# Kernel optimization log

Measured on AMD Instinct MI355X. Metric: run time of the kernel, lower is better.

## Reference

```python
import jax, jax.numpy as jnp
import numpy as np

N_TOKEN = 267735
HEAD = 20000
CUTOFFS = [20000, 20008, 20016, 200000, 267735]  # from cl_root_leaf_dict with 2 roots of 8 leaves
N_ROOTS = 2


def setup_inputs() -> dict:
    key = jax.random.key(0)
    k1, k2, k3, k4 = jax.random.split(key, 4)
    N, D = 1024, 1024
    hidden = jax.random.normal(k1, (N, D), dtype=jnp.float32)
    target = jax.random.randint(k2, (N,), 0, N_TOKEN)
    W = jax.random.normal(k3, (N_TOKEN, D), dtype=jnp.float32) * 0.02
    b = jnp.zeros((N_TOKEN,), dtype=jnp.float32)
    cluster_weight = jax.random.normal(k4, (2, D), dtype=jnp.float32) * 0.02
    cluster_bias = jnp.zeros((2,), dtype=jnp.float32)
    return {"hidden": hidden, "target": target, "W": W, "b": b,
            "cluster_weight": cluster_weight, "cluster_bias": cluster_bias}


def _nll(hidden, target, W, b, cw, cb):
    cutoff_ends = [0] + CUTOFFS
    # head = first 20000 vocab rows + 2 cluster rows (d_proj == d_embed -> no projection)
    head_w = jnp.concatenate([W[:HEAD], cw], axis=0)          # [20002, D]
    head_b = jnp.concatenate([b[:HEAD], cb], axis=0)          # [20002]
    head_lp = jax.nn.log_softmax(hidden @ head_w.T + head_b, axis=-1)  # [N, 20002]
    n_head_cols = head_lp.shape[1]
    rows = jnp.arange(hidden.shape[0])
    # segment 0: target in [0, 20000) -> nll directly from head log-probs
    lp0 = head_lp[rows, jnp.clip(target, 0, HEAD - 1)]
    nll = -lp0  # only valid where target < HEAD; overwritten below otherwise
    for i in range(1, len(CUTOFFS)):
        l, r = cutoff_ends[i], cutoff_ends[i + 1]
        # per-segment tail logits for all tokens (masked combine keeps shapes static)
        tail_lp = jax.nn.log_softmax(hidden @ W[l:r].T + b[l:r], axis=-1)  # [N, r-l]
        # routing column exactly as in the torch code:
        # j = i-1 for root segments, -(i - n_roots) for the two cluster segments
        j = (i - 1) if i <= N_ROOTS else (n_head_cols - (i - N_ROOTS))
        lp_i = head_lp[:, j] + tail_lp[rows, jnp.clip(target - l, 0, r - l - 1)]
        mask = (target >= l) & (target < r)
        nll = jnp.where(mask, -lp_i, nll)
    return nll


def reference(hidden, target, W, b, cluster_weight, cluster_bias):
    return _nll(hidden, target, W, b, cluster_weight, cluster_bias)
```

## Files before the change

kernel.cpp:

```cpp
#include <hip/hip_runtime.h>
#include <hip/hip_bf16.h>

#define D_DIM 1024
#define NTOK 267735
#define NEXT_ 267737
#define HEADN 20000

typedef __attribute__((ext_vector_type(8))) short bf16x8;
typedef __attribute__((ext_vector_type(4))) float f32x4;
typedef __attribute__((ext_vector_type(4))) unsigned uint4v;

__device__ __forceinline__ int seg_of(int c){
  if (c < HEADN)  return 0;
  if (c < 20008)  return 1;
  if (c < 20016)  return 2;
  if (c < 200000) return 3;
  if (c < NTOK)   return 4;
  return 0;
}

__device__ __forceinline__ unsigned pack2(float x, float y){
  __hip_bfloat16 a = __float2bfloat16(x);
  __hip_bfloat16 b = __float2bfloat16(y);
  unsigned short ua = *reinterpret_cast<unsigned short*>(&a);
  unsigned short ub = *reinterpret_cast<unsigned short*>(&b);
  return (unsigned)ua | ((unsigned)ub << 16);
}

#define BM 256
#define BN 128
#define BK 32
#define NTHREADS 512
#define KSTEPS (D_DIM/BK)
#define NPHASE (KSTEPS/2)
#define NCOLT 2092
#define NBLK 8384

#define APRIME_OFF 32768
#define APRIME_BYTES (1024*1024*2)

__device__ __forceinline__ void stage16(const float* g, unsigned short* l){
  __builtin_amdgcn_global_load_lds(
      (const __attribute__((address_space(1))) void*)g,
      (__attribute__((address_space(3))) void*)l, 16, 0, 0);
}

#define CVTPK(d, x, y) asm("v_cvt_pk_bf16_f32 %0, %1, %2" : "=v"(d) : "v"(x), "v"(y))

__global__ void prep_convert(const float* __restrict__ hidden,
                             unsigned short* __restrict__ Ap)
{
  int t = blockIdx.x * blockDim.x + threadIdx.x;
  int r16 = t & 15, kc = (t >> 4) & 127, rb = t >> 11;
  const float4* src = reinterpret_cast<const float4*>(hidden + ((size_t)(rb*16 + r16) * D_DIM + kc*8));
  float4 x = src[0], y = src[1];
  uint4 o;
  o.x = pack2(x.x, x.y); o.y = pack2(x.z, x.w);
  o.z = pack2(y.x, y.y); o.w = pack2(y.z, y.w);
  reinterpret_cast<uint4*>(Ap)[t] = o;
}

__global__ __launch_bounds__(NTHREADS, 1) void gemm_lse_adir(
    const unsigned short* __restrict__ Ap, const float* __restrict__ W,
    const float* __restrict__ bias,   const float* __restrict__ cw,
    const float* __restrict__ cb,     float* __restrict__ accg)
{
  const int b = blockIdx.x;
  const int k8 = b & 7;
  const int sq_ = b >> 3;
  const int xb = sq_ & 3;
  const int yb = (sq_ >> 2) * 8 + k8;
  if (yb >= NCOLT) return;

  __shared__ unsigned short lsB0[2 * BN * 64];
  __shared__ unsigned short lsB1[2 * BN * 64];

  const int tid = threadIdx.x;
  const int rowBase = xb * BM;
  const int colBase = yb * BN;

  const int lane = tid & 63;
  const int wv = tid >> 6;
  const int wm = wv >> 1;
  const int wn = wv & 1;
  const int q  = lane >> 4;
  const int r16 = lane & 15;

  const float* sp;
  {
    int srow = wv*16 + (lane >> 2);
    int c    = (lane & 3) ^ ((srow >> 1) & 3);
    int col  = colBase + srow;
    const float* base = (col < NTOK)  ? (W  + (size_t)col * D_DIM)
                      : (col < NEXT_) ? (cw + (size_t)(col - NTOK) * D_DIM) : W;
    sp = base + c*4;
  }
  const int dstH0 = wv*512;
  const int dstH1 = 4096 + wv*512;

#define STAGE1(Lbuf, kn) do{ \
    stage16(sp + (kn)*BK,      &Lbuf[((kn)&1)*8192 + dstH0]); \
    stage16(sp + (kn)*BK + 16, &Lbuf[((kn)&1)*8192 + dstH1]); }while(0)
#define STAGE2(Lbuf, kn) do{ STAGE1(Lbuf, kn); STAGE1(Lbuf, (kn)+1); }while(0)

  int loO[4], hiO[4];
#pragma unroll
  for (int j=0;j<4;++j){
    int row = wn*64 + j*16 + r16;
    int swz = (row >> 1) & 3;
    int h   = q >> 1;
    loO[j] = h*4096 + row*32 + (((2*q  ) & 3) ^ swz)*8;
    hiO[j] = h*4096 + row*32 + (((2*q+1) & 3) ^ swz)*8;
  }

  const unsigned short* a0 = Ap + (size_t)(xb*16 + wm*4 + 0)*16384 + q*128 + r16*8;
  const unsigned short* a1 = Ap + (size_t)(xb*16 + wm*4 + 1)*16384 + q*128 + r16*8;
  const unsigned short* a2 = Ap + (size_t)(xb*16 + wm*4 + 2)*16384 + q*128 + r16*8;
  const unsigned short* a3 = Ap + (size_t)(xb*16 + wm*4 + 3)*16384 + q*128 + r16*8;

  f32x4 acc[4][4];
#pragma unroll
  for (int i=0;i<4;++i)
#pragma unroll
    for (int j=0;j<4;++j) acc[i][j] = (f32x4){0.f,0.f,0.f,0.f};

#define BFRAG(Lp, j, out) { \
    float4 lo = *reinterpret_cast<const float4*>(&Lp[loO[j]]); \
    float4 hi = *reinterpret_cast<const float4*>(&Lp[hiO[j]]); \
    unsigned u0,u1,u2,u3; \
    CVTPK(u0, lo.x, lo.y); CVTPK(u1, lo.z, lo.w); \
    CVTPK(u2, hi.x, hi.y); CVTPK(u3, hi.z, hi.w); \
    uint4v uu; uu.x=u0; uu.y=u1; uu.z=u2; uu.w=u3; \
    out = __builtin_bit_cast(bf16x8, uu); }

#define KSTEP(Lp, kt) do{ \
    bf16x8 af0 = *reinterpret_cast<const bf16x8*>(a0 + (kt)*512); \
    bf16x8 af1 = *reinterpret_cast<const bf16x8*>(a1 + (kt)*512); \
    bf16x8 af2 = *reinterpret_cast<const bf16x8*>(a2 + (kt)*512); \
    bf16x8 af3 = *reinterpret_cast<const bf16x8*>(a3 + (kt)*512); \
    bf16x8 b0, b1, b2, b3; \
    BFRAG(Lp, 0, b0); BFRAG(Lp, 1, b1); BFRAG(Lp, 2, b2); BFRAG(Lp, 3, b3); \
    acc[0][0] = __builtin_amdgcn_mfma_f32_16x16x32_bf16(af0, b0, acc[0][0], 0,0,0); \
    acc[0][1] = __builtin_amdgcn_mfma_f32_16x16x32_bf16(af0, b1, acc[0][1], 0,0,0); \
    acc[0][2] = __builtin_amdgcn_mfma_f32_16x16x32_bf16(af0, b2, acc[0][2], 0,0,0); \
    acc[0][3] = __builtin_amdgcn_mfma_f32_16x16x32_bf16(af0, b3, acc[0][3], 0,0,0); \
    acc[1][0] = __builtin_amdgcn_mfma_f32_16x16x32_bf16(af1, b0, acc[1][0], 0,0,0); \
    acc[1][1] = __builtin_amdgcn_mfma_f32_16x16x32_bf16(af1, b1, acc[1][1], 0,0,0); \
    acc[1][2] = __builtin_amdgcn_mfma_f32_16x16x32_bf16(af1, b2, acc[1][2], 0,0,0); \
    acc[1][3] = __builtin_amdgcn_mfma_f32_16x16x32_bf16(af1, b3, acc[1][3], 0,0,0); \
    acc[2][0] = __builtin_amdgcn_mfma_f32_16x16x32_bf16(af2, b0, acc[2][0], 0,0,0); \
    acc[2][1] = __builtin_amdgcn_mfma_f32_16x16x32_bf16(af2, b1, acc[2][1], 0,0,0); \
    acc[2][2] = __builtin_amdgcn_mfma_f32_16x16x32_bf16(af2, b2, acc[2][2], 0,0,0); \
    acc[2][3] = __builtin_amdgcn_mfma_f32_16x16x32_bf16(af2, b3, acc[2][3], 0,0,0); \
    acc[3][0] = __builtin_amdgcn_mfma_f32_16x16x32_bf16(af3, b0, acc[3][0], 0,0,0); \
    acc[3][1] = __builtin_amdgcn_mfma_f32_16x16x32_bf16(af3, b1, acc[3][1], 0,0,0); \
    acc[3][2] = __builtin_amdgcn_mfma_f32_16x16x32_bf16(af3, b2, acc[3][2], 0,0,0); \
    acc[3][3] = __builtin_amdgcn_mfma_f32_16x16x32_bf16(af3, b3, acc[3][3], 0,0,0); \
  }while(0)

  STAGE2(lsB0, 0);
  __syncthreads();

  for (int p = 0; p < NPHASE; ++p){
    unsigned short* Lr = (p & 1) ? lsB1 : lsB0;
    unsigned short* Lw = (p & 1) ? lsB0 : lsB1;
    const int k0 = 2*p;

    if (p + 1 < NPHASE) STAGE2(Lw, k0+2);

    KSTEP(Lr,          k0    );
    KSTEP((Lr + 8192), k0 + 1);

    __syncthreads();
  }

  int sq[4]; float bq[4];
#pragma unroll
  for (int f=0; f<4; ++f){
    int c = colBase + wn*64 + f*16 + r16;
    if (c < NTOK)       { sq[f] = seg_of(c); bq[f] = bias[c]; }
    else if (c < NEXT_) { sq[f] = 0;         bq[f] = cb[c - NTOK]; }
    else                { sq[f] = -1;        bq[f] = 0.f; }
  }
  int sfirst = seg_of(colBase);
  int clast  = colBase + BN - 1; if (clast > NEXT_-1) clast = NEXT_-1;
  int slast  = seg_of(clast);
  int smin = sfirst, smax = slast;
  if (slast < sfirst){ smin = 0; smax = 4; }

#pragma unroll
  for (int i=0;i<4;++i){
#pragma unroll
    for (int r=0;r<4;++r){
      float e[4];
#pragma unroll
      for (int f=0;f<4;++f) e[f] = __expf(acc[i][f][r] + bq[f]);
      int rowg = rowBase + wm*64 + i*16 + (lane>>4)*4 + r;
      for (int s2 = smin; s2 <= smax; ++s2){
        float p2 = 0.f;
#pragma unroll
        for (int f=0;f<4;++f) p2 += (sq[f]==s2) ? e[f] : 0.f;
#pragma unroll
        for (int off=1; off<16; off<<=1) p2 += __shfl_xor(p2, off, 16);
        if ((lane & 15) == 0 && p2 != 0.f) atomicAdd(&accg[rowg*8 + s2], p2);
      }
    }
  }
}

__global__ __launch_bounds__(256) void finalize_kernel(
    const float* __restrict__ hidden, const int* __restrict__ target,
    const float* __restrict__ W,      const float* __restrict__ bias,
    const float* __restrict__ cw,     const float* __restrict__ cb,
    const float* __restrict__ accg,   float* __restrict__ out)
{
  const int row  = blockIdx.x * 4 + (threadIdx.x >> 6);
  const int lane = threadIdx.x & 63;
  const int t = target[row];

  const float4* h4 = reinterpret_cast<const float4*>(hidden + (size_t)row * D_DIM);
  const float4* w1 = reinterpret_cast<const float4*>(W + (size_t)t * D_DIM);
  int s = 0; const float* jraw = W; float jb = 0.f;
  if (t >= HEADN){
    if      (t < 20008)  { s=1; jraw = W;          jb = bias[0]; }
    else if (t < 20016)  { s=2; jraw = W + D_DIM;  jb = bias[1]; }
    else if (t < 200000) { s=3; jraw = cw + D_DIM; jb = cb[1];   }
    else                 { s=4; jraw = cw;         jb = cb[0];   }
  }
  const float4* w2 = reinterpret_cast<const float4*>(jraw);

  float p1 = 0.f, p2 = 0.f;
#pragma unroll
  for (int j=0;j<4;++j){
    float4 hv = h4[lane + 64*j];
    float4 av = w1[lane + 64*j];
    float4 bv = w2[lane + 64*j];
    p1 += hv.x*av.x + hv.y*av.y + hv.z*av.z + hv.w*av.w;
    p2 += hv.x*bv.x + hv.y*bv.y + hv.z*bv.z + hv.w*bv.w;
  }
#pragma unroll
  for (int off=32; off; off>>=1){
    p1 += __shfl_xor(p1, off, 64);
    p2 += __shfl_xor(p2, off, 64);
  }

  if (lane == 0){
    float lseH = __logf(accg[row*8 + 0]);
    float nll;
    if (t < HEADN){
      nll = -(p1 + bias[t] - lseH);
    } else {
      float lseS = __logf(accg[row*8 + s]);
      nll = -((p2 + jb - lseH) + (p1 + bias[t] - lseS));
    }
    out[row] = nll;
  }
}

extern "C" void kernel_launch(void* const* d_in, const int* in_sizes, int n_in,
                              void* d_out, int out_size, void* d_ws, size_t ws_size,
                              hipStream_t stream)
{
  const float* hidden = (const float*)d_in[0];
  const int*   target = (const int*)  d_in[1];
  const float* W      = (const float*)d_in[2];
  const float* bias   = (const float*)d_in[3];
  const float* cw     = (const float*)d_in[4];
  const float* cb     = (const float*)d_in[5];
  float* out  = (float*)d_out;
  float* accg = (float*)d_ws;
  unsigned short* Ap = (unsigned short*)((char*)d_ws + APRIME_OFF);

  hipMemsetAsync(accg, 0, 1024*8*sizeof(float), stream);

  prep_convert<<<512, 256, 0, stream>>>(hidden, Ap);
  gemm_lse_adir<<<NBLK, NTHREADS, 0, stream>>>(Ap, W, bias, cw, cb, accg);
  finalize_kernel<<<256, 256, 0, stream>>>(hidden, target, W, bias, cw, cb, accg, out);
}
```

Before: 821.4 us.

## Switch GEMM from 16x16x32 to 32x32x16 MFMA with matching A layout

Replaces the 4x4 grid of 16x16x32 bf16 MFMAs per wave with a 2x2 grid of 32x32x16 MFMAs. The prep kernel's packed bf16 layout of hidden and the LDS fragment offsets for W are reworked to match the new operand shape. The epilogue is rewritten for the 32x32 accumulator layout and reduces over 32 lanes. The aim is fewer MFMA issues and fewer A-fragment loads per k-step. The trade-off is more accumulator registers per MFMA and a wider shuffle reduction in the epilogue.

```diff
diff --git a/kernel.cpp b/kernel.cpp
--- a/kernel.cpp
+++ b/kernel.cpp
@@ -7,7 +7,7 @@
 #define HEADN 20000
 
 typedef __attribute__((ext_vector_type(8))) short bf16x8;
-typedef __attribute__((ext_vector_type(4))) float f32x4;
+typedef __attribute__((ext_vector_type(16))) float f32x16;
 typedef __attribute__((ext_vector_type(4))) unsigned uint4v;
 
 __device__ __forceinline__ int seg_of(int c){
@@ -51,8 +51,10 @@
                              unsigned short* __restrict__ Ap)
 {
   int t = blockIdx.x * blockDim.x + threadIdx.x;
-  int r16 = t & 15, kc = (t >> 4) & 127, rb = t >> 11;
-  const float4* src = reinterpret_cast<const float4*>(hidden + ((size_t)(rb*16 + r16) * D_DIM + kc*8));
+  int l = t & 63, kc = (t >> 6) & 63, rb = t >> 12;
+  int row = rb*32 + (l & 31);
+  int kb  = kc*16 + (l >> 5)*8;
+  const float4* src = reinterpret_cast<const float4*>(hidden + (size_t)row * D_DIM + kb);
   float4 x = src[0], y = src[1];
   uint4 o;
   o.x = pack2(x.x, x.y); o.y = pack2(x.z, x.w);
@@ -83,8 +85,8 @@
   const int wv = tid >> 6;
   const int wm = wv >> 1;
   const int wn = wv & 1;
-  const int q  = lane >> 4;
-  const int r16 = lane & 15;
+  const int l31 = lane & 31;
+  const int lh  = lane >> 5;
 
   const float* sp;
   {
@@ -103,30 +105,26 @@
     stage16(sp + (kn)*BK + 16, &Lbuf[((kn)&1)*8192 + dstH1]); }while(0)
 #define STAGE2(Lbuf, kn) do{ STAGE1(Lbuf, kn); STAGE1(Lbuf, (kn)+1); }while(0)
 
-  int loO[4], hiO[4];
-#pragma unroll
-  for (int j=0;j<4;++j){
-    int row = wn*64 + j*16 + r16;
-    int swz = (row >> 1) & 3;
-    int h   = q >> 1;
-    loO[j] = h*4096 + row*32 + (((2*q  ) & 3) ^ swz)*8;
-    hiO[j] = h*4096 + row*32 + (((2*q+1) & 3) ^ swz)*8;
-  }
-
-  const unsigned short* a0 = Ap + (size_t)(xb*16 + wm*4 + 0)*16384 + q*128 + r16*8;
-  const unsigned short* a1 = Ap + (size_t)(xb*16 + wm*4 + 1)*16384 + q*128 + r16*8;
-  const unsigned short* a2 = Ap + (size_t)(xb*16 + wm*4 + 2)*16384 + q*128 + r16*8;
-  const unsigned short* a3 = Ap + (size_t)(xb*16 + wm*4 + 3)*16384 + q*128 + r16*8;
-
-  f32x4 acc[4][4];
-#pragma unroll
-  for (int i=0;i<4;++i)
-#pragma unroll
-    for (int j=0;j<4;++j) acc[i][j] = (f32x4){0.f,0.f,0.f,0.f};
-
-#define BFRAG(Lp, j, out) { \
-    float4 lo = *reinterpret_cast<const float4*>(&Lp[loO[j]]); \
-    float4 hi = *reinterpret_cast<const float4*>(&Lp[hiO[j]]); \
+  int lo0, hi0, lo1, hi1;
+  {
+    int cn0 = wn*64 + l31;        int swz0 = (cn0 >> 1) & 3;
+    int cn1 = wn*64 + 32 + l31;   int swz1 = (cn1 >> 1) & 3;
+    int c0 = 2*lh;
+    lo0 = cn0*32 + ((c0    ) ^ swz0)*8;
+    hi0 = cn0*32 + ((c0 + 1) ^ swz0)*8;
+    lo1 = cn1*32 + ((c0    ) ^ swz1)*8;
+    hi1 = cn1*32 + ((c0 + 1) ^ swz1)*8;
+  }
+
+  const unsigned short* aB = Ap + (size_t)(xb*8 + wm*2)*32768 + (size_t)lane*8;
+
+  f32x16 acc00, acc01, acc10, acc11;
+#pragma unroll
+  for (int r=0;r<16;++r){ acc00[r]=0.f; acc01[r]=0.f; acc10[r]=0.f; acc11[r]=0.f; }
+
+#define BFRAG32(Lp, oLo, oHi, out) { \
+    float4 lo = *reinterpret_cast<const float4*>(&Lp[oLo]); \
+    float4 hi = *reinterpret_cast<const float4*>(&Lp[oHi]); \
     unsigned u0,u1,u2,u3; \
     CVTPK(u0, lo.x, lo.y); CVTPK(u1, lo.z, lo.w); \
     CVTPK(u2, hi.x, hi.y); CVTPK(u3, hi.z, hi.w); \
@@ -134,28 +132,23 @@
     out = __builtin_bit_cast(bf16x8, uu); }
 
 #define KSTEP(Lp, kt) do{ \
-    bf16x8 af0 = *reinterpret_cast<const bf16x8*>(a0 + (kt)*512); \
-    bf16x8 af1 = *reinterpret_cast<const bf16x8*>(a1 + (kt)*512); \
-    bf16x8 af2 = *reinterpret_cast<const bf16x8*>(a2 + (kt)*512); \
-    bf16x8 af3 = *reinterpret_cast<const bf16x8*>(a3 + (kt)*512); \
-    bf16x8 b0, b1, b2, b3; \
-    BFRAG(Lp, 0, b0); BFRAG(Lp, 1, b1); BFRAG(Lp, 2, b2); BFRAG(Lp, 3, b3); \
-    acc[0][0] = __builtin_amdgcn_mfma_f32_16x16x32_bf16(af0, b0, acc[0][0], 0,0,0); \
-    acc[0][1] = __builtin_amdgcn_mfma_f32_16x16x32_bf16(af0, b1, acc[0][1], 0,0,0); \
-    acc[0][2] = __builtin_amdgcn_mfma_f32_16x16x32_bf16(af0, b2, acc[0][2], 0,0,0); \
-    acc[0][3] = __builtin_amdgcn_mfma_f32_16x16x32_bf16(af0, b3, acc[0][3], 0,0,0); \
-    acc[1][0] = __builtin_amdgcn_mfma_f32_16x16x32_bf16(af1, b0, acc[1][0], 0,0,0); \
-    acc[1][1] = __builtin_amdgcn_mfma_f32_16x16x32_bf16(af1, b1, acc[1][1], 0,0,0); \
-    acc[1][2] = __builtin_amdgcn_mfma_f32_16x16x32_bf16(af1, b2, acc[1][2], 0,0,0); \
-    acc[1][3] = __builtin_amdgcn_mfma_f32_16x16x32_bf16(af1, b3, acc[1][3], 0,0,0); \
-    acc[2][0] = __builtin_amdgcn_mfma_f32_16x16x32_bf16(af2, b0, acc[2][0], 0,0,0); \
-    acc[2][1] = __builtin_amdgcn_mfma_f32_16x16x32_bf16(af2, b1, acc[2][1], 0,0,0); \
-    acc[2][2] = __builtin_amdgcn_mfma_f32_16x16x32_bf16(af2, b2, acc[2][2], 0,0,0); \
-    acc[2][3] = __builtin_amdgcn_mfma_f32_16x16x32_bf16(af2, b3, acc[2][3], 0,0,0); \
-    acc[3][0] = __builtin_amdgcn_mfma_f32_16x16x32_bf16(af3, b0, acc[3][0], 0,0,0); \
-    acc[3][1] = __builtin_amdgcn_mfma_f32_16x16x32_bf16(af3, b1, acc[3][1], 0,0,0); \
-    acc[3][2] = __builtin_amdgcn_mfma_f32_16x16x32_bf16(af3, b2, acc[3][2], 0,0,0); \
-    acc[3][3] = __builtin_amdgcn_mfma_f32_16x16x32_bf16(af3, b3, acc[3][3], 0,0,0); \
+    bf16x8 a00 = *reinterpret_cast<const bf16x8*>(aB +         (2*(kt)  )*512); \
+    bf16x8 a01 = *reinterpret_cast<const bf16x8*>(aB +         (2*(kt)+1)*512); \
+    bf16x8 a10 = *reinterpret_cast<const bf16x8*>(aB + 32768 + (2*(kt)  )*512); \
+    bf16x8 a11 = *reinterpret_cast<const bf16x8*>(aB + 32768 + (2*(kt)+1)*512); \
+    bf16x8 b00, b01, b10, b11; \
+    BFRAG32(Lp, lo0,        hi0,        b00);    \
+    BFRAG32(Lp, lo0 + 4096, hi0 + 4096, b01);    \
+    BFRAG32(Lp, lo1,        hi1,        b10);    \
+    BFRAG32(Lp, lo1 + 4096, hi1 + 4096, b11);    \
+    acc00 = __builtin_amdgcn_mfma_f32_32x32x16_bf16(a00, b00, acc00, 0,0,0); \
+    acc00 = __builtin_amdgcn_mfma_f32_32x32x16_bf16(a01, b01, acc00, 0,0,0); \
+    acc01 = __builtin_amdgcn_mfma_f32_32x32x16_bf16(a00, b10, acc01, 0,0,0); \
+    acc01 = __builtin_amdgcn_mfma_f32_32x32x16_bf16(a01, b11, acc01, 0,0,0); \
+    acc10 = __builtin_amdgcn_mfma_f32_32x32x16_bf16(a10, b00, acc10, 0,0,0); \
+    acc10 = __builtin_amdgcn_mfma_f32_32x32x16_bf16(a11, b01, acc10, 0,0,0); \
+    acc11 = __builtin_amdgcn_mfma_f32_32x32x16_bf16(a10, b10, acc11, 0,0,0); \
+    acc11 = __builtin_amdgcn_mfma_f32_32x32x16_bf16(a11, b11, acc11, 0,0,0); \
   }while(0)
 
   STAGE2(lsB0, 0);
@@ -174,13 +167,16 @@
     __syncthreads();
   }
 
-  int sq[4]; float bq[4];
-#pragma unroll
-  for (int f=0; f<4; ++f){
-    int c = colBase + wn*64 + f*16 + r16;
-    if (c < NTOK)       { sq[f] = seg_of(c); bq[f] = bias[c]; }
-    else if (c < NEXT_) { sq[f] = 0;         bq[f] = cb[c - NTOK]; }
-    else                { sq[f] = -1;        bq[f] = 0.f; }
+  int sq0, sq1; float bq0, bq1;
+  {
+    int c = colBase + wn*64 + l31;
+    if (c < NTOK)       { sq0 = seg_of(c); bq0 = bias[c]; }
+    else if (c < NEXT_) { sq0 = 0;         bq0 = cb[c - NTOK]; }
+    else                { sq0 = -1;        bq0 = 0.f; }
+    int c2 = c + 32;
+    if (c2 < NTOK)       { sq1 = seg_of(c2); bq1 = bias[c2]; }
+    else if (c2 < NEXT_) { sq1 = 0;          bq1 = cb[c2 - NTOK]; }
+    else                 { sq1 = -1;         bq1 = 0.f; }
   }
   int sfirst = seg_of(colBase);
   int clast  = colBase + BN - 1; if (clast > NEXT_-1) clast = NEXT_-1;
@@ -188,24 +184,23 @@
   int smin = sfirst, smax = slast;
   if (slast < sfirst){ smin = 0; smax = 4; }
 
-#pragma unroll
-  for (int i=0;i<4;++i){
-#pragma unroll
-    for (int r=0;r<4;++r){
-      float e[4];
-#pragma unroll
-      for (int f=0;f<4;++f) e[f] = __expf(acc[i][f][r] + bq[f]);
-      int rowg = rowBase + wm*64 + i*16 + (lane>>4)*4 + r;
-      for (int s2 = smin; s2 <= smax; ++s2){
-        float p2 = 0.f;
-#pragma unroll
-        for (int f=0;f<4;++f) p2 += (sq[f]==s2) ? e[f] : 0.f;
-#pragma unroll
-        for (int off=1; off<16; off<<=1) p2 += __shfl_xor(p2, off, 16);
-        if ((lane & 15) == 0 && p2 != 0.f) atomicAdd(&accg[rowg*8 + s2], p2);
-      }
-    }
-  }
+#define EPIROW(AC0, AC1, MT, RG) { \
+    float e0 = __expf(AC0[RG] + bq0); \
+    float e1 = __expf(AC1[RG] + bq1); \
+    int rowg = rowBase + wm*64 + MT*32 + ((RG)&3) + 8*((RG)>>2) + 4*lh; \
+    for (int s2 = smin; s2 <= smax; ++s2){ \
+      float pp = ((sq0==s2) ? e0 : 0.f) + ((sq1==s2) ? e1 : 0.f); \
+      pp += __shfl_xor(pp, 1, 32);  pp += __shfl_xor(pp, 2, 32); \
+      pp += __shfl_xor(pp, 4, 32);  pp += __shfl_xor(pp, 8, 32); \
+      pp += __shfl_xor(pp, 16, 32); \
+      if (l31 == 0 && pp != 0.f) atomicAdd(&accg[rowg*8 + s2], pp); \
+    } }
+
+#pragma unroll
+  for (int rg = 0; rg < 16; ++rg){ EPIROW(acc00, acc01, 0, rg); }
+#pragma unroll
+  for (int rg = 0; rg < 16; ++rg){ EPIROW(acc10, acc11, 1, rg); }
+
 }
 
 __global__ __launch_bounds__(256) void finalize_kernel(
```

Measured after the change: 924.3 us. 1.13x slower.

## Group rows by target segment and skip GEMM tiles with no matching rows

Applied to the files above, without the earlier changes.

A new single-block kernel buckets the 1024 rows by target vocabulary segment and builds a permutation, its inverse and per-segment row ranges. It also zeroes the accumulators, replacing the separate memset. The BF16 conversion now writes rows in the permuted order. The GEMM+LSE kernel returns early for column tiles whose tail segment has no rows in that tile's row block, so tail logits are only computed for rows that need them. This adds one tiny serial launch plus indirect row gathers, in exchange for skipping a large share of the vocabulary GEMM.

```diff
diff --git a/kernel.cpp b/kernel.cpp
--- a/kernel.cpp
+++ b/kernel.cpp
@@ -36,7 +36,10 @@
 #define NCOLT 2092
 #define NBLK 8384
 
-#define APRIME_OFF 32768
+#define PERM_OFF   32768
+#define IPERM_OFF  36864
+#define SEGB_OFF   40960
+#define APRIME_OFF 65536
 #define APRIME_BYTES (1024*1024*2)
 
 __device__ __forceinline__ void stage16(const float* g, unsigned short* l){
@@ -47,12 +50,37 @@
 
 #define CVTPK(d, x, y) asm("v_cvt_pk_bf16_f32 %0, %1, %2" : "=v"(d) : "v"(x), "v"(y))
 
+__global__ void sort_kernel(const int* __restrict__ target,
+                            float* __restrict__ accg,
+                            int* __restrict__ perm, int* __restrict__ iperm,
+                            int* __restrict__ segB)
+{
+  __shared__ int cnt[5]; __shared__ int base[5];
+  int t = threadIdx.x;
+  if (t < 5) cnt[t] = 0;
+  __syncthreads();
+  for (int i=0;i<8;++i) accg[t*8+i] = 0.f;
+  int s = seg_of(target[t]);
+  int pos = atomicAdd(&cnt[s], 1);
+  __syncthreads();
+  if (t == 0){
+    int acc = 0;
+    for (int q=0;q<5;++q){ base[q]=acc; segB[q*2]=acc; acc+=cnt[q]; segB[q*2+1]=acc; }
+  }
+  __syncthreads();
+  int slot = base[s] + pos;
+  perm[slot] = t;
+  iperm[t]   = slot;
+}
+
 __global__ void prep_convert(const float* __restrict__ hidden,
+                             const int* __restrict__ perm,
                              unsigned short* __restrict__ Ap)
 {
   int t = blockIdx.x * blockDim.x + threadIdx.x;
   int r16 = t & 15, kc = (t >> 4) & 127, rb = t >> 11;
-  const float4* src = reinterpret_cast<const float4*>(hidden + ((size_t)(rb*16 + r16) * D_DIM + kc*8));
+  int row = perm[rb*16 + r16];
+  const float4* src = reinterpret_cast<const float4*>(hidden + ((size_t)row * D_DIM + kc*8));
   float4 x = src[0], y = src[1];
   uint4 o;
   o.x = pack2(x.x, x.y); o.y = pack2(x.z, x.w);
@@ -63,7 +91,8 @@
 __global__ __launch_bounds__(NTHREADS, 1) void gemm_lse_adir(
     const unsigned short* __restrict__ Ap, const float* __restrict__ W,
     const float* __restrict__ bias,   const float* __restrict__ cw,
-    const float* __restrict__ cb,     float* __restrict__ accg)
+    const float* __restrict__ cb,     float* __restrict__ accg,
+    const int* __restrict__ segB)
 {
   const int b = blockIdx.x;
   const int k8 = b & 7;
@@ -72,12 +101,27 @@
   const int yb = (sq_ >> 2) * 8 + k8;
   if (yb >= NCOLT) return;
 
+  const int rowBase = xb * BM;
+  const int colBase = yb * BN;
+
+  {
+    int cfirst = colBase;
+    int clast  = colBase + BN - 1; if (clast > NEXT_-1) clast = NEXT_-1;
+    bool need = (clast >= NTOK) || (cfirst < HEADN);
+    if (!need){
+      int sf = seg_of(cfirst), sl = seg_of(clast < NTOK ? clast : NTOK-1);
+      for (int s = sf; s <= sl && !need; ++s){
+        if (s == 0) need = true;
+        else if (segB[2*s] < rowBase + BM && segB[2*s+1] > rowBase) need = true;
+      }
+    }
+    if (!need) return;
+  }
+
   __shared__ unsigned short lsB0[2 * BN * 64];
   __shared__ unsigned short lsB1[2 * BN * 64];
 
   const int tid = threadIdx.x;
-  const int rowBase = xb * BM;
-  const int colBase = yb * BN;
 
   const int lane = tid & 63;
   const int wv = tid >> 6;
@@ -212,11 +256,13 @@
     const float* __restrict__ hidden, const int* __restrict__ target,
     const float* __restrict__ W,      const float* __restrict__ bias,
     const float* __restrict__ cw,     const float* __restrict__ cb,
-    const float* __restrict__ accg,   float* __restrict__ out)
+    const float* __restrict__ accg,   const int* __restrict__ iperm,
+    float* __restrict__ out)
 {
   const int row  = blockIdx.x * 4 + (threadIdx.x >> 6);
   const int lane = threadIdx.x & 63;
   const int t = target[row];
+  const int slot = iperm[row];
 
   const float4* h4 = reinterpret_cast<const float4*>(hidden + (size_t)row * D_DIM);
   const float4* w1 = reinterpret_cast<const float4*>(W + (size_t)t * D_DIM);
@@ -245,12 +291,12 @@
   }
 
   if (lane == 0){
-    float lseH = __logf(accg[row*8 + 0]);
+    float lseH = __logf(accg[slot*8 + 0]);
     float nll;
     if (t < HEADN){
       nll = -(p1 + bias[t] - lseH);
     } else {
-      float lseS = __logf(accg[row*8 + s]);
+      float lseS = __logf(accg[slot*8 + s]);
       nll = -((p2 + jb - lseH) + (p1 + bias[t] - lseS));
     }
     out[row] = nll;
@@ -269,11 +315,13 @@
   const float* cb     = (const float*)d_in[5];
   float* out  = (float*)d_out;
   float* accg = (float*)d_ws;
+  int*   perm  = (int*)((char*)d_ws + PERM_OFF);
+  int*   iperm = (int*)((char*)d_ws + IPERM_OFF);
+  int*   segB  = (int*)((char*)d_ws + SEGB_OFF);
   unsigned short* Ap = (unsigned short*)((char*)d_ws + APRIME_OFF);
 
-  hipMemsetAsync(accg, 0, 1024*8*sizeof(float), stream);
-
-  prep_convert<<<512, 256, 0, stream>>>(hidden, Ap);
-  gemm_lse_adir<<<NBLK, NTHREADS, 0, stream>>>(Ap, W, bias, cw, cb, accg);
-  finalize_kernel<<<256, 256, 0, stream>>>(hidden, target, W, bias, cw, cb, accg, out);
-}
+  sort_kernel<<<1, 1024, 0, stream>>>(target, accg, perm, iperm, segB);
+  prep_convert<<<512, 256, 0, stream>>>(hidden, perm, Ap);
+  gemm_lse_adir<<<NBLK, NTHREADS, 0, stream>>>(Ap, W, bias, cw, cb, accg, segB);
+  finalize_kernel<<<256, 256, 0, stream>>>(hidden, target, W, bias, cw, cb, accg, iperm, out);
+}
```

Result: no change. 826.6 us (+0.6%).
